# Kernel tuning notes

Hardware: AMD Instinct MI355X
Metric: run time of the kernel (lower is better)

Reference implementation:

```python
import jax, jax.numpy as jnp
import numpy as np


def setup_inputs() -> dict:
    key = jax.random.key(0)
    k = jax.random.split(key, 4)
    B, D, H, W, C = 4, 64, 64, 64, 64
    R = 16  # reduction ratio
    KS = 7
    x = jax.random.normal(k[0], (B, D, H, W, C), dtype=jnp.float32)
    w1 = jax.random.normal(k[1], (C, C // R), dtype=jnp.float32) * (2.0 / C) ** 0.5
    b1 = jnp.zeros((C // R,), dtype=jnp.float32)
    w2 = jax.random.normal(k[2], (C // R, C), dtype=jnp.float32) * (2.0 / (C // R)) ** 0.5
    b2 = jnp.zeros((C,), dtype=jnp.float32)
    conv_w = jax.random.normal(k[3], (KS, KS, KS, 2, 1), dtype=jnp.float32) * (2.0 / (KS ** 3 * 2)) ** 0.5
    return {"x": x, "w1": w1, "b1": b1, "w2": w2, "b2": b2, "conv_w": conv_w}


def _mlp(v, w1, b1, w2, b2):
    # shared two-layer MLP: relu then sigmoid
    h = jax.nn.relu(v @ w1 + b1)
    return jax.nn.sigmoid(h @ w2 + b2)


def reference(x, w1, b1, w2, b2, conv_w):
    # ---- channel attention ----
    avg_pool = jnp.mean(x, axis=(1, 2, 3))          # [B, C]
    max_pool = jnp.max(x, axis=(1, 2, 3))           # [B, C]
    ca = _mlp(avg_pool, w1, b1, w2, b2) + _mlp(max_pool, w1, b1, w2, b2)  # [B, C]
    channel_refined = x * ca[:, None, None, None, :]  # [B, D, H, W, C]
    # ---- spatial attention ----
    avg_sp = jnp.mean(channel_refined, axis=-1, keepdims=True)  # [B,D,H,W,1]
    max_sp = jnp.max(channel_refined, axis=-1, keepdims=True)   # [B,D,H,W,1]
    concat = jnp.concatenate([avg_sp, max_sp], axis=-1)          # [B,D,H,W,2]
    sa = jax.lax.conv_general_dilated(
        concat, conv_w,
        window_strides=(1, 1, 1), padding="SAME",
        dimension_numbers=("NDHWC", "DHWIO", "NDHWC"),
    )  # [B,D,H,W,1]
    sa = jax.nn.sigmoid(sa)
    return channel_refined * sa
```

## Files before the change

kernel.cpp:

```cpp
#include <hip/hip_runtime.h>
#include <hip/hip_fp16.h>
#include <math.h>

#define BATCH 4
#define SPATIAL (64*64*64)
#define NB 512

typedef float f32x4 __attribute__((ext_vector_type(4)));
typedef unsigned int u32x4 __attribute__((ext_vector_type(4)));

__device__ __forceinline__ float sigmoidf_(float z) { return 1.f / (1.f + expf(-z)); }

template<bool W16>
__global__ __launch_bounds__(256) void pool_partial_kernel(
    const float* __restrict__ x, __half* __restrict__ x16,
    float* __restrict__ psum, float* __restrict__ pmax) {
  const int b     = blockIdx.x / NB;
  const int chunk = blockIdx.x % NB;
  const int tid  = threadIdx.x;
  const int w    = tid >> 6;
  const int lane = tid & 63;
  const int q    = lane >> 4;
  const int g    = lane & 15;

  const f32x4* xb = (const f32x4*)x + (size_t)b * SPATIAL * 16;
  uint2* x16b = (uint2*)x16 + (size_t)b * SPATIAL * 16;

  float s0=0.f, s1=0.f, s2=0.f, s3=0.f;
  float m0=-INFINITY, m1=-INFINITY, m2=-INFINITY, m3=-INFINITY;

  const int PPB = SPATIAL / NB;
  #pragma unroll 4
  for (int i = 0; i < PPB / 16; ++i) {
    int p = chunk * PPB + i * 16 + w * 4 + q;
    size_t gi = (size_t)p * 16 + g;
    f32x4 v;
    if (W16) v = __builtin_nontemporal_load(xb + gi);
    else     v = xb[gi];
    if (W16) {
      union { __half2 h[2]; uint2 u; } pk;
      pk.h[0] = __floats2half2_rn(v.x, v.y);
      pk.h[1] = __floats2half2_rn(v.z, v.w);
      x16b[gi] = pk.u;
    }
    s0 += v.x; s1 += v.y; s2 += v.z; s3 += v.w;
    m0 = fmaxf(m0, v.x); m1 = fmaxf(m1, v.y); m2 = fmaxf(m2, v.z); m3 = fmaxf(m3, v.w);
  }
  #pragma unroll
  for (int mask = 16; mask <= 32; mask <<= 1) {
    s0 += __shfl_xor(s0, mask); s1 += __shfl_xor(s1, mask);
    s2 += __shfl_xor(s2, mask); s3 += __shfl_xor(s3, mask);
    m0 = fmaxf(m0, __shfl_xor(m0, mask)); m1 = fmaxf(m1, __shfl_xor(m1, mask));
    m2 = fmaxf(m2, __shfl_xor(m2, mask)); m3 = fmaxf(m3, __shfl_xor(m3, mask));
  }
  __shared__ float lsum[4][64];
  __shared__ float lmax[4][64];
  if (q == 0) {
    lsum[w][g*4+0] = s0; lsum[w][g*4+1] = s1; lsum[w][g*4+2] = s2; lsum[w][g*4+3] = s3;
    lmax[w][g*4+0] = m0; lmax[w][g*4+1] = m1; lmax[w][g*4+2] = m2; lmax[w][g*4+3] = m3;
  }
  __syncthreads();
  if (tid < 64) {
    float s = lsum[0][tid] + lsum[1][tid] + lsum[2][tid] + lsum[3][tid];
    float m = fmaxf(fmaxf(lmax[0][tid], lmax[1][tid]), fmaxf(lmax[2][tid], lmax[3][tid]));
    psum[((size_t)b * NB + chunk) * 64 + tid] = s;
    pmax[((size_t)b * NB + chunk) * 64 + tid] = m;
  }
}

__global__ __launch_bounds__(256) void ca_kernel(
    const float* __restrict__ psum, const float* __restrict__ pmax,
    const float* __restrict__ w1, const float* __restrict__ b1,
    const float* __restrict__ w2, const float* __restrict__ b2,
    float* __restrict__ ca) {
  const int b = blockIdx.x;
  const int tid = threadIdx.x;
  const int r = tid >> 6, c = tid & 63;
  float s = 0.f, m = -INFINITY;
  #pragma unroll 4
  for (int k = r; k < NB; k += 4) {
    s += psum[((size_t)b * NB + k) * 64 + c];
    m = fmaxf(m, pmax[((size_t)b * NB + k) * 64 + c]);
  }
  __shared__ float ls[4][64];
  __shared__ float lm[4][64];
  ls[r][c] = s; lm[r][c] = m;
  __syncthreads();
  if (tid < 64) {
    const int cc = tid;
    float ss = ls[0][cc] + ls[1][cc] + ls[2][cc] + ls[3][cc];
    float mm = fmaxf(fmaxf(lm[0][cc], lm[1][cc]), fmaxf(lm[2][cc], lm[3][cc]));
    float avg = ss * (1.f / SPATIAL);

    float w1c[4];
    #pragma unroll
    for (int j = 0; j < 4; ++j) w1c[j] = w1[cc * 4 + j];
    float pa[4], pm[4];
    #pragma unroll
    for (int j = 0; j < 4; ++j) { pa[j] = avg * w1c[j]; pm[j] = mm * w1c[j]; }
    #pragma unroll
    for (int mask = 1; mask < 64; mask <<= 1) {
      #pragma unroll
      for (int j = 0; j < 4; ++j) {
        pa[j] += __shfl_xor(pa[j], mask);
        pm[j] += __shfl_xor(pm[j], mask);
      }
    }
    float za = b2[cc], zm = b2[cc];
    #pragma unroll
    for (int j = 0; j < 4; ++j) {
      float ha = fmaxf(pa[j] + b1[j], 0.f);
      float hm = fmaxf(pm[j] + b1[j], 0.f);
      za += ha * w2[j * 64 + cc];
      zm += hm * w2[j * 64 + cc];
    }
    ca[b * 64 + cc] = sigmoidf_(za) + sigmoidf_(zm);
  }
}

__global__ __launch_bounds__(256) void spstats16_kernel(
    const __half* __restrict__ x16, const float* __restrict__ ca, __half2* __restrict__ sp) {
  const int tid = threadIdx.x, lane = tid & 63, w = tid >> 6;
  const int q = lane >> 3, g = lane & 7;
  const int waveId = blockIdx.x * 4 + w;
  const int nWaves = gridDim.x * 4;
  const int NGRP = BATCH * SPATIAL / 8;
  const u32x4* x4 = (const u32x4*)x16;
  for (int grp = waveId; grp < NGRP; grp += nWaves) {
    int p = grp * 8 + q;
    int b = p >> 18;
    union { u32x4 v; unsigned u[4]; } uu;
    uu.v = x4[(size_t)p * 8 + g];
    const float* cab = ca + b * 64 + g * 8;
    f32x4 c0 = *(const f32x4*)cab;
    f32x4 c1 = *(const f32x4*)(cab + 4);
    float2 f0 = __half22float2(*(__half2*)&uu.u[0]);
    float2 f1 = __half22float2(*(__half2*)&uu.u[1]);
    float2 f2 = __half22float2(*(__half2*)&uu.u[2]);
    float2 f3 = __half22float2(*(__half2*)&uu.u[3]);
    float a0 = f0.x*c0.x, a1 = f0.y*c0.y, a2 = f1.x*c0.z, a3 = f1.y*c0.w;
    float a4 = f2.x*c1.x, a5 = f2.y*c1.y, a6 = f3.x*c1.z, a7 = f3.y*c1.w;
    float s = ((a0+a1)+(a2+a3)) + ((a4+a5)+(a6+a7));
    float m = fmaxf(fmaxf(fmaxf(a0,a1),fmaxf(a2,a3)), fmaxf(fmaxf(a4,a5),fmaxf(a6,a7)));
    #pragma unroll
    for (int mask = 1; mask < 8; mask <<= 1) {
      s += __shfl_xor(s, mask);
      m = fmaxf(m, __shfl_xor(m, mask));
    }
    if (g == 0) sp[p] = __floats2half2_rn(s * (1.f / 64.f), m);
  }
}

__global__ __launch_bounds__(256) void spstats_kernel(
    const float* __restrict__ x, const float* __restrict__ ca, __half2* __restrict__ sp) {
  const int tid = threadIdx.x, lane = tid & 63, w = tid >> 6;
  const int q = lane >> 4, g = lane & 15;
  const int waveId = blockIdx.x * 4 + w;
  const int nWaves = gridDim.x * 4;
  const int NGRP = BATCH * SPATIAL / 4;
  const float4* x4  = (const float4*)x;
  const float4* ca4 = (const float4*)ca;
  for (int grp = waveId; grp < NGRP; grp += nWaves) {
    int p = grp * 4 + q;
    int b = p >> 18;
    float4 v  = x4[(size_t)p * 16 + g];
    float4 cv = ca4[b * 16 + g];
    float ax = v.x * cv.x, ay = v.y * cv.y, az = v.z * cv.z, aw = v.w * cv.w;
    float s = ax + ay + az + aw;
    float m = fmaxf(fmaxf(ax, ay), fmaxf(az, aw));
    #pragma unroll
    for (int mask = 1; mask < 16; mask <<= 1) {
      s += __shfl_xor(s, mask);
      m = fmaxf(m, __shfl_xor(m, mask));
    }
    if (g == 0) sp[p] = __floats2half2_rn(s * (1.f / 64.f), m);
  }
}

#define CZT 8
#define CYT 2
#define CPL (CZT + 6)
#define CRW (CYT + 6)
#define CXW 70
template<bool X16>
__global__ __launch_bounds__(256) void conv_final_kernel(
    const __half2* __restrict__ sp, const float* __restrict__ cw,
    const float* __restrict__ x, const __half* __restrict__ x16,
    const float* __restrict__ ca, float* __restrict__ out) {
  __shared__ __half2 tile[CPL * CRW * CXW];

  const int bid = blockIdx.x;
  const int zg = bid & 7;
  const int yg = (bid >> 3) & 31;
  const int b  = bid >> 8;
  const int z0 = zg * CZT;
  const int y0 = yg * CYT;

  const __half2* spb = sp + (size_t)b * SPATIAL;

  const int NE = CPL * CRW * CXW;
  for (int e = threadIdx.x; e < NE; e += 256) {
    int pl  = e / (CRW * CXW);
    int rem = e - pl * (CRW * CXW);
    int row = rem / CXW;
    int xi  = rem - row * CXW;
    int z = z0 + pl - 3;
    int y = y0 + row - 3;
    int xx = xi - 3;
    __half2 v = __floats2half2_rn(0.f, 0.f);
    if ((unsigned)z < 64u && (unsigned)y < 64u && (unsigned)xx < 64u)
      v = spb[(z << 12) + (y << 6) + xx];
    tile[e] = v;
  }
  __syncthreads();

  const int lane = threadIdx.x & 63;
  const int ty   = threadIdx.x >> 6;
  const int zb   = ty * 2;

  float acc[2][2] = {{0.f, 0.f}, {0.f, 0.f}};

  for (int pp = 0; pp < 8; ++pp) {
    const int pl = zb + pp;
    #pragma unroll
    for (int ry = 0; ry < 8; ++ry) {
      const __half2* rowp = tile + (pl * CRW + ry) * CXW + lane;
      float fx[7], fy[7];
      #pragma unroll
      for (int k = 0; k < 7; ++k) {
        float2 f = __half22float2(rowp[k]);
        fx[k] = f.x; fy[k] = f.y;
      }
      #pragma unroll
      for (int dz = 0; dz < 2; ++dz) {
        const int kz = pp - dz;
        if ((unsigned)kz > 6u) continue;
        #pragma unroll
        for (int dy = 0; dy < 2; ++dy) {
          const int ky = ry - dy;
          if ((unsigned)ky > 6u) continue;
          const float* wp = cw + (kz * 49 + ky * 7) * 2;
          float a = acc[dz][dy];
          #pragma unroll
          for (int kx = 0; kx < 7; ++kx)
            a = fmaf(fx[kx], wp[kx * 2], fmaf(fy[kx], wp[kx * 2 + 1], a));
          acc[dz][dy] = a;
        }
      }
    }
  }

  if (X16) {
    const float4* ca4 = (const float4*)ca;
    const float4 cav = ca4[b * 16 + (lane & 15)];
    const uint2* xr = (const uint2*)x16;
    #pragma unroll
    for (int dz = 0; dz < 2; ++dz) {
      #pragma unroll
      for (int dy = 0; dy < 2; ++dy) {
        const float s_own = sigmoidf_(acc[dz][dy]);
        const int z = z0 + zb + dz;
        const int y = y0 + dy;
        const size_t base = (((size_t)b * 64 + z) * 64 + y) * 1024;
        #pragma unroll 4
        for (int k = 0; k < 16; ++k) {
          const int f = lane + k * 64;
          const float sv = __shfl(s_own, (lane >> 4) + k * 4);
          uint2 u = xr[base + f];
          float2 t0 = __half22float2(*(__half2*)&u.x);
          float2 t1 = __half22float2(*(__half2*)&u.y);
          f32x4 o;
          o.x = t0.x * cav.x * sv; o.y = t0.y * cav.y * sv;
          o.z = t1.x * cav.z * sv; o.w = t1.y * cav.w * sv;
          __builtin_nontemporal_store(o, (f32x4*)out + base + f);
        }
      }
    }
  } else {
    const float4* x4 = (const float4*)x;
    const float4* ca4 = (const float4*)ca;
    const float4 cav = ca4[b * 16 + (lane & 15)];
    #pragma unroll
    for (int dz = 0; dz < 2; ++dz) {
      #pragma unroll
      for (int dy = 0; dy < 2; ++dy) {
        const float s_own = sigmoidf_(acc[dz][dy]);
        const int z = z0 + zb + dz;
        const int y = y0 + dy;
        const size_t base = (((size_t)b * 64 + z) * 64 + y) * 1024;
        #pragma unroll 4
        for (int k = 0; k < 16; ++k) {
          const int f = lane + k * 64;
          const float sv = __shfl(s_own, (lane >> 4) + k * 4);
          float4 v = x4[base + f];
          f32x4 o;
          o.x = v.x * cav.x * sv; o.y = v.y * cav.y * sv;
          o.z = v.z * cav.z * sv; o.w = v.w * cav.w * sv;
          __builtin_nontemporal_store(o, (f32x4*)(out + (base + f) * 4));
        }
      }
    }
  }
}

extern "C" void kernel_launch(void* const* d_in, const int* in_sizes, int n_in,
                              void* d_out, int out_size, void* d_ws, size_t ws_size,
                              hipStream_t stream) {
  const float* x  = (const float*)d_in[0];
  const float* w1 = (const float*)d_in[1];
  const float* b1 = (const float*)d_in[2];
  const float* w2 = (const float*)d_in[3];
  const float* b2 = (const float*)d_in[4];
  const float* cw = (const float*)d_in[5];
  float* out = (float*)d_out;

  const size_t x16_bytes = (size_t)BATCH * SPATIAL * 64 * 2;
  const size_t sp_bytes  = (size_t)BATCH * SPATIAL * 4;
  const size_t red_bytes = (size_t)BATCH * NB * 64 * 4;
  const size_t need = x16_bytes + sp_bytes + 2 * red_bytes + 1024;

  if (ws_size >= need) {
    __half*  x16  = (__half*)d_ws;
    __half2* sp   = (__half2*)((char*)d_ws + x16_bytes);
    float*   psum = (float*)((char*)sp + sp_bytes);
    float*   pmax = psum + (size_t)BATCH * NB * 64;
    float*   ca   = pmax + (size_t)BATCH * NB * 64;

    pool_partial_kernel<true><<<BATCH * NB, 256, 0, stream>>>(x, x16, psum, pmax);
    ca_kernel<<<BATCH, 256, 0, stream>>>(psum, pmax, w1, b1, w2, b2, ca);
    spstats16_kernel<<<2048, 256, 0, stream>>>(x16, ca, sp);
    conv_final_kernel<true><<<BATCH * 32 * 8, 256, 0, stream>>>(sp, cw, x, x16, ca, out);
  } else {
    __half2* sp   = (__half2*)d_ws;
    float*   psum = (float*)((char*)sp + sp_bytes);
    float*   pmax = psum + (size_t)BATCH * NB * 64;
    float*   ca   = pmax + (size_t)BATCH * NB * 64;

    pool_partial_kernel<false><<<BATCH * NB, 256, 0, stream>>>(x, nullptr, psum, pmax);
    ca_kernel<<<BATCH, 256, 0, stream>>>(psum, pmax, w1, b1, w2, b2, ca);
    spstats_kernel<<<2048, 256, 0, stream>>>(x, ca, sp);
    conv_final_kernel<false><<<BATCH * 32 * 8, 256, 0, stream>>>(sp, cw, x, nullptr, ca, out);
  }
}
```

Measured before the change: 212.8 us.

## Use packed half2 FMA for spatial conv and transpose pool partials

The 7x7x7 spatial conv inner loop now runs packed half-precision FMAs (__hfma2) on the half2 tile. It uses weights pre-converted to half2 in the channel-attention kernel, and each z-plane's partial sums are flushed to fp32 accumulators. The pooling partials are stored channel-major, so the CA reduction reads contiguous float4 vectors. Several unroll factors are also raised. Accumulating in fp16 halves the FMA count but loses precision in the conv result.

Result: faster. 182.8 us (-14.1%).

```diff
diff --git a/kernel.cpp b/kernel.cpp
--- a/kernel.cpp
+++ b/kernel.cpp
@@ -30,7 +30,7 @@
   float m0=-INFINITY, m1=-INFINITY, m2=-INFINITY, m3=-INFINITY;
 
   const int PPB = SPATIAL / NB;
-  #pragma unroll 4
+  #pragma unroll 8
   for (int i = 0; i < PPB / 16; ++i) {
     int p = chunk * PPB + i * 16 + w * 4 + q;
     size_t gi = (size_t)p * 16 + g;
@@ -63,8 +63,8 @@
   if (tid < 64) {
     float s = lsum[0][tid] + lsum[1][tid] + lsum[2][tid] + lsum[3][tid];
     float m = fmaxf(fmaxf(lmax[0][tid], lmax[1][tid]), fmaxf(lmax[2][tid], lmax[3][tid]));
-    psum[((size_t)b * NB + chunk) * 64 + tid] = s;
-    pmax[((size_t)b * NB + chunk) * 64 + tid] = m;
+    psum[((size_t)b * 64 + tid) * NB + chunk] = s;
+    pmax[((size_t)b * 64 + tid) * NB + chunk] = m;
   }
 }
 
@@ -72,15 +72,23 @@
     const float* __restrict__ psum, const float* __restrict__ pmax,
     const float* __restrict__ w1, const float* __restrict__ b1,
     const float* __restrict__ w2, const float* __restrict__ b2,
+    const float* __restrict__ cw, __half2* __restrict__ w16,
     float* __restrict__ ca) {
   const int b = blockIdx.x;
   const int tid = threadIdx.x;
+  for (int wi = tid; wi < 343; wi += 256)
+    w16[wi] = __floats2half2_rn(cw[wi * 2], cw[wi * 2 + 1]);
+
   const int r = tid >> 6, c = tid & 63;
+  const f32x4* ps4 = (const f32x4*)(psum + ((size_t)b * 64 + c) * NB + r * 128);
+  const f32x4* pm4 = (const f32x4*)(pmax + ((size_t)b * 64 + c) * NB + r * 128);
   float s = 0.f, m = -INFINITY;
-  #pragma unroll 4
-  for (int k = r; k < NB; k += 4) {
-    s += psum[((size_t)b * NB + k) * 64 + c];
-    m = fmaxf(m, pmax[((size_t)b * NB + k) * 64 + c]);
+  #pragma unroll 8
+  for (int j = 0; j < 32; ++j) {
+    f32x4 vs = ps4[j];
+    f32x4 vm = pm4[j];
+    s += (vs.x + vs.y) + (vs.z + vs.w);
+    m = fmaxf(m, fmaxf(fmaxf(vm.x, vm.y), fmaxf(vm.z, vm.w)));
   }
   __shared__ float ls[4][64];
   __shared__ float lm[4][64];
@@ -184,7 +192,7 @@
 #define CXW 70
 template<bool X16>
 __global__ __launch_bounds__(256) void conv_final_kernel(
-    const __half2* __restrict__ sp, const float* __restrict__ cw,
+    const __half2* __restrict__ sp, const __half2* __restrict__ w16,
     const float* __restrict__ x, const __half* __restrict__ x16,
     const float* __restrict__ ca, float* __restrict__ out) {
   __shared__ __half2 tile[CPL * CRW * CXW];
@@ -218,19 +226,18 @@
   const int ty   = threadIdx.x >> 6;
   const int zb   = ty * 2;
 
-  float acc[2][2] = {{0.f, 0.f}, {0.f, 0.f}};
-
+  float accf[2][2] = {{0.f, 0.f}, {0.f, 0.f}};
+
+  const __half2 zero2 = __floats2half2_rn(0.f, 0.f);
   for (int pp = 0; pp < 8; ++pp) {
     const int pl = zb + pp;
+    __half2 a00 = zero2, a01 = zero2, a10 = zero2, a11 = zero2;
     #pragma unroll
     for (int ry = 0; ry < 8; ++ry) {
       const __half2* rowp = tile + (pl * CRW + ry) * CXW + lane;
-      float fx[7], fy[7];
-      #pragma unroll
-      for (int k = 0; k < 7; ++k) {
-        float2 f = __half22float2(rowp[k]);
-        fx[k] = f.x; fy[k] = f.y;
-      }
+      __half2 h[7];
+      #pragma unroll
+      for (int k = 0; k < 7; ++k) h[k] = rowp[k];
       #pragma unroll
       for (int dz = 0; dz < 2; ++dz) {
         const int kz = pp - dz;
@@ -239,15 +246,20 @@
         for (int dy = 0; dy < 2; ++dy) {
           const int ky = ry - dy;
           if ((unsigned)ky > 6u) continue;
-          const float* wp = cw + (kz * 49 + ky * 7) * 2;
-          float a = acc[dz][dy];
+          const __half2* wp = w16 + kz * 49 + ky * 7;
+          __half2 a = (dz == 0) ? (dy == 0 ? a00 : a01) : (dy == 0 ? a10 : a11);
           #pragma unroll
           for (int kx = 0; kx < 7; ++kx)
-            a = fmaf(fx[kx], wp[kx * 2], fmaf(fy[kx], wp[kx * 2 + 1], a));
-          acc[dz][dy] = a;
+            a = __hfma2(h[kx], wp[kx], a);
+          if (dz == 0) { if (dy == 0) a00 = a; else a01 = a; }
+          else         { if (dy == 0) a10 = a; else a11 = a; }
         }
       }
     }
+    accf[0][0] += __low2float(a00) + __high2float(a00);
+    accf[0][1] += __low2float(a01) + __high2float(a01);
+    accf[1][0] += __low2float(a10) + __high2float(a10);
+    accf[1][1] += __low2float(a11) + __high2float(a11);
   }
 
   if (X16) {
@@ -258,11 +270,11 @@
     for (int dz = 0; dz < 2; ++dz) {
       #pragma unroll
       for (int dy = 0; dy < 2; ++dy) {
-        const float s_own = sigmoidf_(acc[dz][dy]);
+        const float s_own = sigmoidf_(accf[dz][dy]);
         const int z = z0 + zb + dz;
         const int y = y0 + dy;
         const size_t base = (((size_t)b * 64 + z) * 64 + y) * 1024;
-        #pragma unroll 4
+        #pragma unroll 8
         for (int k = 0; k < 16; ++k) {
           const int f = lane + k * 64;
           const float sv = __shfl(s_own, (lane >> 4) + k * 4);
@@ -284,11 +296,11 @@
     for (int dz = 0; dz < 2; ++dz) {
       #pragma unroll
       for (int dy = 0; dy < 2; ++dy) {
-        const float s_own = sigmoidf_(acc[dz][dy]);
+        const float s_own = sigmoidf_(accf[dz][dy]);
         const int z = z0 + zb + dz;
         const int y = y0 + dy;
         const size_t base = (((size_t)b * 64 + z) * 64 + y) * 1024;
-        #pragma unroll 4
+        #pragma unroll 8
         for (int k = 0; k < 16; ++k) {
           const int f = lane + k * 64;
           const float sv = __shfl(s_own, (lane >> 4) + k * 4);
@@ -317,7 +329,8 @@
   const size_t x16_bytes = (size_t)BATCH * SPATIAL * 64 * 2;
   const size_t sp_bytes  = (size_t)BATCH * SPATIAL * 4;
   const size_t red_bytes = (size_t)BATCH * NB * 64 * 4;
-  const size_t need = x16_bytes + sp_bytes + 2 * red_bytes + 1024;
+  const size_t tail_bytes = 256 * 4 + 344 * 4 + 1024;
+  const size_t need = x16_bytes + sp_bytes + 2 * red_bytes + tail_bytes;
 
   if (ws_size >= need) {
     __half*  x16  = (__half*)d_ws;
@@ -325,20 +338,22 @@
     float*   psum = (float*)((char*)sp + sp_bytes);
     float*   pmax = psum + (size_t)BATCH * NB * 64;
     float*   ca   = pmax + (size_t)BATCH * NB * 64;
+    __half2* w16  = (__half2*)(ca + 256);
 
     pool_partial_kernel<true><<<BATCH * NB, 256, 0, stream>>>(x, x16, psum, pmax);
-    ca_kernel<<<BATCH, 256, 0, stream>>>(psum, pmax, w1, b1, w2, b2, ca);
+    ca_kernel<<<BATCH, 256, 0, stream>>>(psum, pmax, w1, b1, w2, b2, cw, w16, ca);
     spstats16_kernel<<<2048, 256, 0, stream>>>(x16, ca, sp);
-    conv_final_kernel<true><<<BATCH * 32 * 8, 256, 0, stream>>>(sp, cw, x, x16, ca, out);
+    conv_final_kernel<true><<<BATCH * 32 * 8, 256, 0, stream>>>(sp, w16, x, x16, ca, out);
   } else {
     __half2* sp   = (__half2*)d_ws;
     float*   psum = (float*)((char*)sp + sp_bytes);
     float*   pmax = psum + (size_t)BATCH * NB * 64;
     float*   ca   = pmax + (size_t)BATCH * NB * 64;
+    __half2* w16  = (__half2*)(ca + 256);
 
     pool_partial_kernel<false><<<BATCH * NB, 256, 0, stream>>>(x, nullptr, psum, pmax);
-    ca_kernel<<<BATCH, 256, 0, stream>>>(psum, pmax, w1, b1, w2, b2, ca);
+    ca_kernel<<<BATCH, 256, 0, stream>>>(psum, pmax, w1, b1, w2, b2, cw, w16, ca);
     spstats_kernel<<<2048, 256, 0, stream>>>(x, ca, sp);
-    conv_final_kernel<false><<<BATCH * 32 * 8, 256, 0, stream>>>(sp, cw, x, nullptr, ca, out);
-  }
-}
+    conv_final_kernel<false><<<BATCH * 32 * 8, 256, 0, stream>>>(sp, w16, x, nullptr, ca, out);
+  }
+}
```
